# Performance work log

Hardware: AMD Instinct MI355X
Metric: run time of the kernel (lower is better)

Reference implementation:

```python
import jax, jax.numpy as jnp
import numpy as np

K = 3            # kernel_size
PAD = K // 2
CENTER_OFFSET = 0.0


def obb2offset(obb, stride):
    """obb: [N,5,H,W] (x_ctr,y_ctr,w,h,theta) in image coords -> deform offsets [N,2*K*K,H,W]."""
    N, _, H, W = obb.shape
    idx = jnp.arange(-PAD, PAD + 1, dtype=jnp.float32)
    yy, xx = jnp.meshgrid(idx, idx, indexing='ij')   # torch.meshgrid default 'ij'
    xx = xx.reshape(-1)                               # [KK]
    yy = yy.reshape(-1)
    x_ctr, y_ctr, w, h, a = [obb[:, i] for i in range(5)]   # each [N,H,W]
    s = jnp.float32(stride)
    x_ctr, y_ctr, w, h = x_ctr / s, y_ctr / s, w / s, h / s
    cos, sin = jnp.cos(a), jnp.sin(a)
    dw, dh = w / K, h / K
    px = dw[..., None] * xx                           # [N,H,W,KK]
    py = dh[..., None] * yy
    xr = cos[..., None] * px - sin[..., None] * py    # rotate kernel grid by theta
    yr = sin[..., None] * px + cos[..., None] * py
    x_anchor = xr + x_ctr[..., None]
    y_anchor = yr + y_ctr[..., None]
    xc = jnp.arange(W, dtype=jnp.float32)
    yc = jnp.arange(H, dtype=jnp.float32)
    x_conv = xc[None, None, :, None] + xx + CENTER_OFFSET   # [1,1,W,KK]
    y_conv = yc[None, :, None, None] + yy + CENTER_OFFSET   # [1,H,1,KK]
    off = jnp.stack([y_anchor - y_conv, x_anchor - x_conv], axis=-1)  # [N,H,W,KK,2]
    return off.reshape(N, H, W, 2 * K * K).transpose(0, 3, 1, 2)


def deform_conv(x, offsets, weight):
    """Deformable conv v1, zero padding, stride 1. x:[N,Cin,H,W], offsets:[N,2KK,H,W], weight:[Cout,Cin,K,K]."""
    N, Cin, H, W = x.shape
    KK = K * K
    Cout = weight.shape[0]
    off = offsets.reshape(N, KK, 2, H, W)
    dy, dx = off[:, :, 0], off[:, :, 1]                        # [N,KK,H,W]
    ky = jnp.arange(KK, dtype=jnp.float32) // K - PAD
    kx = jnp.arange(KK, dtype=jnp.float32) % K - PAD
    py = jnp.arange(H, dtype=jnp.float32)[None, None, :, None] + ky[None, :, None, None] + dy
    px = jnp.arange(W, dtype=jnp.float32)[None, None, None, :] + kx[None, :, None, None] + dx
    y0 = jnp.floor(py)
    x0 = jnp.floor(px)
    ly = py - y0                                               # bilinear fractions
    lx = px - x0
    y0i = y0.astype(jnp.int32)
    x0i = x0.astype(jnp.int32)
    x_flat = x.reshape(N, Cin, H * W)

    def corner(iy, ix):
        valid = (iy >= 0) & (iy < H) & (ix >= 0) & (ix < W)
        idx = jnp.clip(iy, 0, H - 1) * W + jnp.clip(ix, 0, W - 1)  # [N,KK,H,W]
        g = jax.vmap(lambda xf, ii: xf[:, ii.reshape(-1)].reshape(Cin, KK, H, W))(x_flat, idx)
        return jnp.where(valid[:, None], g, 0.0)               # [N,Cin,KK,H,W]

    v00 = corner(y0i, x0i)
    v01 = corner(y0i, x0i + 1)
    v10 = corner(y0i + 1, x0i)
    v11 = corner(y0i + 1, x0i + 1)
    wy = ly[:, None]
    wx = lx[:, None]
    sampled = (v00 * (1 - wy) * (1 - wx) + v01 * (1 - wy) * wx
               + v10 * wy * (1 - wx) + v11 * wy * wx)          # [N,Cin,KK,H,W]
    return jnp.einsum('nckhw,ock->nohw', sampled, weight.reshape(Cout, Cin, KK))


def setup_inputs() -> dict:
    key = jax.random.key(0)
    k1, k2, k3, k4, k5, k6 = jax.random.split(key, 6)
    N, Cin, Cout, H, W, stride = 2, 256, 256, 128, 128, 8
    x = jax.random.normal(k1, (N, Cin, H, W), jnp.float32)
    gy, gx = jnp.meshgrid(jnp.arange(H, dtype=jnp.float32), jnp.arange(W, dtype=jnp.float32), indexing='ij')
    xc = (gx[None] + jax.random.uniform(k2, (N, H, W), minval=-0.5, maxval=0.5)) * stride
    yc = (gy[None] + jax.random.uniform(k3, (N, H, W), minval=-0.5, maxval=0.5)) * stride
    wb = jax.random.uniform(k4, (N, H, W), minval=2.0 * stride, maxval=8.0 * stride)
    hb = jax.random.uniform(k5, (N, H, W), minval=2.0 * stride, maxval=8.0 * stride)
    th = jax.random.uniform(k6, (N, H, W), minval=-np.pi / 2, maxval=np.pi / 2)
    obb = jnp.stack([xc, yc, wb, hb, th], axis=1)              # [N,5,H,W]
    weight = jax.random.normal(jax.random.fold_in(key, 7), (Cout, Cin, K, K), jnp.float32) * 0.02
    return {"x": x, "obb": obb, "weight": weight, "stride": stride}


def reference(x, obb, weight, stride):
    offsets = obb2offset(jax.lax.stop_gradient(obb), stride)   # offsets.detach() in original
    return deform_conv(x, offsets, weight)
```

## Files before the change

### kernel.cpp

```cpp
#include <hip/hip_runtime.h>

#define HH 128
#define WW 128
#define CIN 256
#define COUT 256
#define KTOT 2304
#define HW (HH * WW)
#define NIT 36

typedef __attribute__((ext_vector_type(8))) short short8;
typedef __attribute__((ext_vector_type(4))) float f32x4;

__device__ __forceinline__ unsigned rne_bf16(float f) {
  unsigned u = __float_as_uint(f);
  return (u + 0x7FFFu + ((u >> 16) & 1u)) >> 16;
}
__device__ __forceinline__ unsigned pack_bf16x2(float lo, float hi) {
  return rne_bf16(lo) | (rne_bf16(hi) << 16);
}
__device__ __forceinline__ unsigned cvt_pk_bf16(float lo, float hi) {
  unsigned r;
  asm("v_cvt_pk_bf16_f32 %0, %1, %2" : "=v"(r) : "v"(lo), "v"(hi));
  return r;
}
__device__ __forceinline__ float bflo(unsigned u) { return __uint_as_float(u << 16); }
__device__ __forceinline__ float bfhi(unsigned u) { return __uint_as_float(u & 0xFFFF0000u); }

__device__ __forceinline__ unsigned blend2(unsigned a, unsigned b, unsigned c, unsigned d,
                                           float w00, float w01, float w10, float w11) {
  float lo = w00 * bflo(a) + w01 * bflo(b) + w10 * bflo(c) + w11 * bflo(d);
  float hi = w00 * bfhi(a) + w01 * bfhi(b) + w10 * bfhi(c) + w11 * bfhi(d);
  return cvt_pk_bf16(lo, hi);
}

__device__ __forceinline__ void glds16(const unsigned short* g, unsigned short* l) {
  __builtin_amdgcn_global_load_lds(
      (const __attribute__((address_space(1))) void*)g,
      (__attribute__((address_space(3))) void*)l, 16, 0, 0);
}

__global__ void prep_inputs(const float* __restrict__ x, const float* __restrict__ wsrc,
                            unsigned short* __restrict__ xt, unsigned short* __restrict__ wT) {
  int b = blockIdx.x;
  __shared__ float tile[64][129];
  if (b < 1024) {
    int cg = b & 3;
    int nh = b >> 2;
    int n = nh >> 7, h = nh & 127;
    int c0 = cg << 6;
    const float* xp = x + ((size_t)n * CIN * HH + h) * WW;
    for (int e = threadIdx.x; e < 64 * 128; e += 256) {
      int w = e & 127, ci = e >> 7;
      tile[ci][w] = xp[(size_t)(c0 + ci) * HW + w];
    }
    __syncthreads();
    unsigned* dst = (unsigned*)(xt + ((size_t)(n * HH + h) * WW) * CIN + c0);
    for (int e = threadIdx.x; e < 128 * 32; e += 256) {
      int w = e >> 5, cp = e & 31;
      dst[w * (CIN / 2) + cp] = pack_bf16x2(tile[2 * cp][w], tile[2 * cp + 1][w]);
    }
  } else {
    int o = (b - 1024) * 256 + threadIdx.x;
    if (o >= COUT * KTOT) return;
    int co = o / KTOT;
    int r = o - co * KTOT;
    int kk = r >> 8, ci = r & 255;
    wT[o] = rne_bf16(wsrc[(size_t)(co * CIN + ci) * 9 + kk]);
  }
}

__global__ __launch_bounds__(512, 2) void fused_deform_gemm(
    const float* __restrict__ obb, const unsigned short* __restrict__ xt,
    const unsigned short* __restrict__ wT, float* __restrict__ out,
    const int* __restrict__ stride_p) {
  int g = blockIdx.x;
  int xcd = g & 7, li = g >> 3;
  int u = xcd * 64 + li;
  int mh = u & 1;
  int bm = u >> 1;
  int n = bm >> 7, h = bm & 127;
  int tid = threadIdx.x;

  __shared__ __align__(16) unsigned short Alds[64 * 64];
  __shared__ __align__(16) unsigned short Blds[256 * 64];
  __shared__ float pcx[64], pcy[64], pA[64], pB[64], pC[64], pD[64];

  float inv_s = 1.0f / (float)stride_p[0];

  if (tid < 64) {
    int w = mh * 64 + tid;
    const float* op = obb + ((size_t)n * 5 * HH + h) * WW + w;
    float xc = op[0] * inv_s;
    float yc = op[(size_t)1 * HW] * inv_s;
    float bw = op[(size_t)2 * HW] * inv_s;
    float bh = op[(size_t)3 * HW] * inv_s;
    float th = op[(size_t)4 * HW];
    float sn, cs;
    sincosf(th, &sn, &cs);
    float dw = bw * (1.0f / 3.0f), dh = bh * (1.0f / 3.0f);
    pcx[tid] = xc; pcy[tid] = yc;
    pA[tid] = dw * cs; pB[tid] = dh * sn;
    pC[tid] = dw * sn; pD[tid] = dh * cs;
  }

  f32x4 acc[2][4] = {};

  int lane = tid & 63;
  int wv = tid >> 6;
  int wm = (wv & 1) * 32;
  int wn = (wv >> 1) * 64;
  int l15 = lane & 15, l4 = lane >> 4;

  int chunk8 = (lane & 7) * 8;
  int p = wv * 8 + (lane >> 3);
  int AldsOff = p * 128 + (((lane & 7) * 16) ^ ((p & 7) << 4));

  int cbl = ((lane & 7) * 16) ^ ((lane >> 3) << 4);
  int BsrcC[4];
  int BldsC[4];
#pragma unroll
  for (int t = 0; t < 4; ++t) {
    int row = t * 64 + wv * 8 + (lane >> 3);
    BsrcC[t] = row * (KTOT * 2) + cbl;
    BldsC[t] = (t * 64 + wv * 8) * 128;
  }

  int rdXor = (l15 & 7) << 4;
  int rc0 = (l4 * 16) ^ rdXor;
  int rc1 = (64 + l4 * 16) ^ rdXor;

  float wgt_[4];
  int boff[4];
  uint4 pf[4];
  uint4 aw;

  __syncthreads();

  auto prep = [&](int kk) {
    float fky = (float)(kk / 3 - 1);
    float fkx = (float)(kk % 3 - 1);
    float sx = pcx[p] + fkx * pA[p] - fky * pB[p];
    float sy = pcy[p] + fkx * pC[p] + fky * pD[p];
    float fx = floorf(sx), fy = floorf(sy);
    float lx = sx - fx, ly = sy - fy;
    int x0 = (int)fx, y0 = (int)fy;
    float vy0 = (y0 >= 0 && y0 < HH) ? 1.0f : 0.0f;
    float vy1 = (y0 >= -1 && y0 < HH - 1) ? 1.0f : 0.0f;
    float vx0 = (x0 >= 0 && x0 < WW) ? 1.0f : 0.0f;
    float vx1 = (x0 >= -1 && x0 < WW - 1) ? 1.0f : 0.0f;
    wgt_[0] = (1.0f - ly) * (1.0f - lx) * vy0 * vx0;
    wgt_[1] = (1.0f - ly) * lx * vy0 * vx1;
    wgt_[2] = ly * (1.0f - lx) * vy1 * vx0;
    wgt_[3] = ly * lx * vy1 * vx1;
    int xc0 = min(max(x0, 0), WW - 1), xc1 = min(max(x0 + 1, 0), WW - 1);
    int yc0 = min(max(y0, 0), HH - 1), yc1 = min(max(y0 + 1, 0), HH - 1);
    int rb0 = (n * HH + yc0) * WW, rb1 = (n * HH + yc1) * WW;
    boff[0] = (rb0 + xc0) * CIN;
    boff[1] = (rb0 + xc1) * CIN;
    boff[2] = (rb1 + xc0) * CIN;
    boff[3] = (rb1 + xc1) * CIN;
  };

  auto issueA = [&](int cc) {
    int co = cc * 64 + chunk8;
#pragma unroll
    for (int c = 0; c < 4; ++c)
      pf[c] = *(const uint4*)(xt + boff[c] + co);
  };

  auto blendA = [&]() {
    uint4 r;
    r.x = blend2(pf[0].x, pf[1].x, pf[2].x, pf[3].x, wgt_[0], wgt_[1], wgt_[2], wgt_[3]);
    r.y = blend2(pf[0].y, pf[1].y, pf[2].y, pf[3].y, wgt_[0], wgt_[1], wgt_[2], wgt_[3]);
    r.z = blend2(pf[0].z, pf[1].z, pf[2].z, pf[3].z, wgt_[0], wgt_[1], wgt_[2], wgt_[3]);
    r.w = blend2(pf[0].w, pf[1].w, pf[2].w, pf[3].w, wgt_[0], wgt_[1], wgt_[2], wgt_[3]);
    aw = r;
  };

  prep(0);
  issueA(0);
  blendA();
  issueA(1);

  char* AB = (char*)Alds;
  char* BB = (char*)Blds;

  for (int it = 0; it < NIT; ++it) {
    *(uint4*)(AB + AldsOff) = aw;
    {
      const unsigned short* wTit = wT + it * 64;
#pragma unroll
      for (int t = 0; t < 4; ++t)
        glds16((const unsigned short*)((const char*)wTit + BsrcC[t]),
               (unsigned short*)(BB + BldsC[t]));
    }
    asm volatile("s_waitcnt vmcnt(0) lgkmcnt(0)" ::: "memory");
    __builtin_amdgcn_s_barrier();
    asm volatile("" ::: "memory");

    int nx = it + 1;
    if (nx < NIT) {
      blendA();
      int nn = it + 2;
      if (nn < NIT) {
        if ((nn & 3) == 0) prep(nn >> 2);
        issueA(nn & 3);
      }
    }

#pragma unroll
    for (int ksi = 0; ksi < 2; ++ksi) {
      int rc = ksi ? rc1 : rc0;
      short8 af[2];
#pragma unroll
      for (int i = 0; i < 2; ++i)
        af[i] = *(const short8*)(AB + (wm + i * 16 + l15) * 128 + rc);
#pragma unroll
      for (int j = 0; j < 4; ++j) {
        short8 bf = *(const short8*)(BB + (wn + j * 16 + l15) * 128 + rc);
#pragma unroll
        for (int i = 0; i < 2; ++i)
          acc[i][j] = __builtin_amdgcn_mfma_f32_16x16x32_bf16(af[i], bf, acc[i][j], 0, 0, 0);
      }
    }
    asm volatile("s_waitcnt lgkmcnt(0)" ::: "memory");
    __builtin_amdgcn_s_barrier();
    asm volatile("" ::: "memory");
  }

  float* outp = out + (size_t)n * COUT * HW + (size_t)h * WW + mh * 64;
#pragma unroll
  for (int i = 0; i < 2; ++i) {
    int w0 = wm + i * 16 + l4 * 4;
#pragma unroll
    for (int j = 0; j < 4; ++j) {
      int co = wn + j * 16 + l15;
      *(f32x4*)(outp + (size_t)co * HW + w0) = acc[i][j];
    }
  }
}

extern "C" void kernel_launch(void* const* d_in, const int* in_sizes, int n_in,
                              void* d_out, int out_size, void* d_ws, size_t ws_size,
                              hipStream_t stream) {
  const float* x = (const float*)d_in[0];
  const float* obb = (const float*)d_in[1];
  const float* wgt = (const float*)d_in[2];
  const int* stridep = (const int*)d_in[3];
  float* out = (float*)d_out;

  unsigned short* xt = (unsigned short*)d_ws;
  unsigned short* wT = xt + (size_t)2 * HH * WW * CIN;

  prep_inputs<<<dim3(1024 + 2304), 256, 0, stream>>>(x, wgt, xt, wT);
  fused_deform_gemm<<<dim3(512), 512, 0, stream>>>(obb, xt, wT, out, stridep);
}
```

Measured before the change: 153.2 us.

## Load weights directly into MFMA registers and double-buffer A tile in LDS

Pre-permutes the bf16 weights into an MFMA fragment-ready layout so each wave loads its B operands straight from global memory into registers, with no LDS staging. This removes the B LDS buffer and one barrier per iteration. The A tile is double-buffered in LDS, per-pixel OBB parameters are kept in registers instead of shared memory, and the bilinear blend uses packed f32 FMA. Launch bounds are raised to 4 blocks, which trades register pressure and repeated global weight reads for higher occupancy and less synchronisation.

```diff
diff --git a/kernel.cpp b/kernel.cpp
--- a/kernel.cpp
+++ b/kernel.cpp
@@ -10,6 +10,7 @@
 
 typedef __attribute__((ext_vector_type(8))) short short8;
 typedef __attribute__((ext_vector_type(4))) float f32x4;
+typedef __attribute__((ext_vector_type(2))) float f32x2;
 
 __device__ __forceinline__ unsigned rne_bf16(float f) {
   unsigned u = __float_as_uint(f);
@@ -23,24 +24,25 @@
   asm("v_cvt_pk_bf16_f32 %0, %1, %2" : "=v"(r) : "v"(lo), "v"(hi));
   return r;
 }
-__device__ __forceinline__ float bflo(unsigned u) { return __uint_as_float(u << 16); }
-__device__ __forceinline__ float bfhi(unsigned u) { return __uint_as_float(u & 0xFFFF0000u); }
-
-__device__ __forceinline__ unsigned blend2(unsigned a, unsigned b, unsigned c, unsigned d,
-                                           float w00, float w01, float w10, float w11) {
-  float lo = w00 * bflo(a) + w01 * bflo(b) + w10 * bflo(c) + w11 * bflo(d);
-  float hi = w00 * bfhi(a) + w01 * bfhi(b) + w10 * bfhi(c) + w11 * bfhi(d);
-  return cvt_pk_bf16(lo, hi);
-}
-
-__device__ __forceinline__ void glds16(const unsigned short* g, unsigned short* l) {
-  __builtin_amdgcn_global_load_lds(
-      (const __attribute__((address_space(1))) void*)g,
-      (__attribute__((address_space(3))) void*)l, 16, 0, 0);
+__device__ __forceinline__ f32x2 up2(unsigned u) {
+  f32x2 r;
+  r.x = __uint_as_float(u << 16);
+  r.y = __uint_as_float(u & 0xFFFF0000u);
+  return r;
+}
+__device__ __forceinline__ f32x2 pkmul(f32x2 w, f32x2 v) {
+  f32x2 d;
+  asm("v_pk_mul_f32 %0, %1, %2" : "=v"(d) : "v"(w), "v"(v));
+  return d;
+}
+__device__ __forceinline__ f32x2 pkfma(f32x2 w, f32x2 v, f32x2 c) {
+  f32x2 d;
+  asm("v_pk_fma_f32 %0, %1, %2, %3" : "=v"(d) : "v"(w), "v"(v), "v"(c));
+  return d;
 }
 
 __global__ void prep_inputs(const float* __restrict__ x, const float* __restrict__ wsrc,
-                            unsigned short* __restrict__ xt, unsigned short* __restrict__ wT) {
+                            unsigned short* __restrict__ xt, unsigned short* __restrict__ wB) {
   int b = blockIdx.x;
   __shared__ float tile[64][129];
   if (b < 1024) {
@@ -65,13 +67,19 @@
     int co = o / KTOT;
     int r = o - co * KTOT;
     int kk = r >> 8, ci = r & 255;
-    wT[o] = rne_bf16(wsrc[(size_t)(co * CIN + ci) * 9 + kk]);
-  }
-}
-
-__global__ __launch_bounds__(512, 2) void fused_deform_gemm(
+    int it = r >> 6;
+    int rem = r & 63;
+    int ksi = rem >> 5;
+    int l4 = (rem >> 3) & 3;
+    int e = rem & 7;
+    int off = (it * 32 + (co >> 4) * 2 + ksi) * 512 + (l4 * 16 + (co & 15)) * 8 + e;
+    wB[off] = rne_bf16(wsrc[(size_t)(co * CIN + ci) * 9 + kk]);
+  }
+}
+
+__global__ __launch_bounds__(512, 4) void fused_deform_gemm(
     const float* __restrict__ obb, const unsigned short* __restrict__ xt,
-    const unsigned short* __restrict__ wT, float* __restrict__ out,
+    const unsigned short* __restrict__ wB, float* __restrict__ out,
     const int* __restrict__ stride_p) {
   int g = blockIdx.x;
   int xcd = g & 7, li = g >> 3;
@@ -81,14 +89,23 @@
   int n = bm >> 7, h = bm & 127;
   int tid = threadIdx.x;
 
-  __shared__ __align__(16) unsigned short Alds[64 * 64];
-  __shared__ __align__(16) unsigned short Blds[256 * 64];
-  __shared__ float pcx[64], pcy[64], pA[64], pB[64], pC[64], pD[64];
+  __shared__ __align__(16) unsigned short Alds[2][64 * 64];
 
   float inv_s = 1.0f / (float)stride_p[0];
 
-  if (tid < 64) {
-    int w = mh * 64 + tid;
+  int lane = tid & 63;
+  int wv = tid >> 6;
+  int wm = (wv & 1) * 32;
+  int wn = (wv >> 1) * 64;
+  int l15 = lane & 15, l4 = lane >> 4;
+
+  int chunk8 = (lane & 7) * 8;
+  int p = wv * 8 + (lane >> 3);
+  int AldsOff = p * 128 + (((lane & 7) * 16) ^ ((p & 7) << 4));
+
+  float cx_, cy_, pa_, pb_, pc_, pd_;
+  {
+    int w = mh * 64 + p;
     const float* op = obb + ((size_t)n * 5 * HH + h) * WW + w;
     float xc = op[0] * inv_s;
     float yc = op[(size_t)1 * HW] * inv_s;
@@ -98,49 +115,29 @@
     float sn, cs;
     sincosf(th, &sn, &cs);
     float dw = bw * (1.0f / 3.0f), dh = bh * (1.0f / 3.0f);
-    pcx[tid] = xc; pcy[tid] = yc;
-    pA[tid] = dw * cs; pB[tid] = dh * sn;
-    pC[tid] = dw * sn; pD[tid] = dh * cs;
+    cx_ = xc; cy_ = yc;
+    pa_ = dw * cs; pb_ = dh * sn;
+    pc_ = dw * sn; pd_ = dh * cs;
   }
 
   f32x4 acc[2][4] = {};
 
-  int lane = tid & 63;
-  int wv = tid >> 6;
-  int wm = (wv & 1) * 32;
-  int wn = (wv >> 1) * 64;
-  int l15 = lane & 15, l4 = lane >> 4;
-
-  int chunk8 = (lane & 7) * 8;
-  int p = wv * 8 + (lane >> 3);
-  int AldsOff = p * 128 + (((lane & 7) * 16) ^ ((p & 7) << 4));
-
-  int cbl = ((lane & 7) * 16) ^ ((lane >> 3) << 4);
-  int BsrcC[4];
-  int BldsC[4];
-#pragma unroll
-  for (int t = 0; t < 4; ++t) {
-    int row = t * 64 + wv * 8 + (lane >> 3);
-    BsrcC[t] = row * (KTOT * 2) + cbl;
-    BldsC[t] = (t * 64 + wv * 8) * 128;
-  }
+  const char* wBb = (const char*)wB + ((wv >> 1) * 4) * 2048 + lane * 16;
 
   int rdXor = (l15 & 7) << 4;
   int rc0 = (l4 * 16) ^ rdXor;
   int rc1 = (64 + l4 * 16) ^ rdXor;
 
-  float wgt_[4];
+  f32x2 wgt2[4];
   int boff[4];
   uint4 pf[4];
   uint4 aw;
 
-  __syncthreads();
-
   auto prep = [&](int kk) {
     float fky = (float)(kk / 3 - 1);
     float fkx = (float)(kk % 3 - 1);
-    float sx = pcx[p] + fkx * pA[p] - fky * pB[p];
-    float sy = pcy[p] + fkx * pC[p] + fky * pD[p];
+    float sx = cx_ + fkx * pa_ - fky * pb_;
+    float sy = cy_ + fkx * pc_ + fky * pd_;
     float fx = floorf(sx), fy = floorf(sy);
     float lx = sx - fx, ly = sy - fy;
     int x0 = (int)fx, y0 = (int)fy;
@@ -148,10 +145,14 @@
     float vy1 = (y0 >= -1 && y0 < HH - 1) ? 1.0f : 0.0f;
     float vx0 = (x0 >= 0 && x0 < WW) ? 1.0f : 0.0f;
     float vx1 = (x0 >= -1 && x0 < WW - 1) ? 1.0f : 0.0f;
-    wgt_[0] = (1.0f - ly) * (1.0f - lx) * vy0 * vx0;
-    wgt_[1] = (1.0f - ly) * lx * vy0 * vx1;
-    wgt_[2] = ly * (1.0f - lx) * vy1 * vx0;
-    wgt_[3] = ly * lx * vy1 * vx1;
+    float w00 = (1.0f - ly) * (1.0f - lx) * vy0 * vx0;
+    float w01 = (1.0f - ly) * lx * vy0 * vx1;
+    float w10 = ly * (1.0f - lx) * vy1 * vx0;
+    float w11 = ly * lx * vy1 * vx1;
+    wgt2[0] = (f32x2){w00, w00};
+    wgt2[1] = (f32x2){w01, w01};
+    wgt2[2] = (f32x2){w10, w10};
+    wgt2[3] = (f32x2){w11, w11};
     int xc0 = min(max(x0, 0), WW - 1), xc1 = min(max(x0 + 1, 0), WW - 1);
     int yc0 = min(max(y0, 0), HH - 1), yc1 = min(max(y0 + 1, 0), HH - 1);
     int rb0 = (n * HH + yc0) * WW, rb1 = (n * HH + yc1) * WW;
@@ -168,61 +169,70 @@
       pf[c] = *(const uint4*)(xt + boff[c] + co);
   };
 
+  auto blendW = [&](unsigned a, unsigned b, unsigned c, unsigned d) -> unsigned {
+    f32x2 s = pkmul(wgt2[0], up2(a));
+    s = pkfma(wgt2[1], up2(b), s);
+    s = pkfma(wgt2[2], up2(c), s);
+    s = pkfma(wgt2[3], up2(d), s);
+    return cvt_pk_bf16(s.x, s.y);
+  };
+
   auto blendA = [&]() {
     uint4 r;
-    r.x = blend2(pf[0].x, pf[1].x, pf[2].x, pf[3].x, wgt_[0], wgt_[1], wgt_[2], wgt_[3]);
-    r.y = blend2(pf[0].y, pf[1].y, pf[2].y, pf[3].y, wgt_[0], wgt_[1], wgt_[2], wgt_[3]);
-    r.z = blend2(pf[0].z, pf[1].z, pf[2].z, pf[3].z, wgt_[0], wgt_[1], wgt_[2], wgt_[3]);
-    r.w = blend2(pf[0].w, pf[1].w, pf[2].w, pf[3].w, wgt_[0], wgt_[1], wgt_[2], wgt_[3]);
+    r.x = blendW(pf[0].x, pf[1].x, pf[2].x, pf[3].x);
+    r.y = blendW(pf[0].y, pf[1].y, pf[2].y, pf[3].y);
+    r.z = blendW(pf[0].z, pf[1].z, pf[2].z, pf[3].z);
+    r.w = blendW(pf[0].w, pf[1].w, pf[2].w, pf[3].w);
     aw = r;
   };
+
+  char* AB = (char*)&Alds[0][0];
 
   prep(0);
   issueA(0);
   blendA();
+  *(uint4*)(AB + AldsOff) = aw;
   issueA(1);
-
-  char* AB = (char*)Alds;
-  char* BB = (char*)Blds;
+  asm volatile("s_waitcnt lgkmcnt(0)" ::: "memory");
+  __builtin_amdgcn_s_barrier();
+  asm volatile("" ::: "memory");
 
   for (int it = 0; it < NIT; ++it) {
-    *(uint4*)(AB + AldsOff) = aw;
-    {
-      const unsigned short* wTit = wT + it * 64;
-#pragma unroll
-      for (int t = 0; t < 4; ++t)
-        glds16((const unsigned short*)((const char*)wTit + BsrcC[t]),
-               (unsigned short*)(BB + BldsC[t]));
-    }
-    asm volatile("s_waitcnt vmcnt(0) lgkmcnt(0)" ::: "memory");
-    __builtin_amdgcn_s_barrier();
-    asm volatile("" ::: "memory");
-
-    int nx = it + 1;
-    if (nx < NIT) {
+    const char* bp = wBb + it * 32768;
+    short8 bf[8];
+#pragma unroll
+    for (int j = 0; j < 4; ++j) {
+      bf[j * 2 + 0] = *(const short8*)(bp + j * 2048);
+      bf[j * 2 + 1] = *(const short8*)(bp + j * 2048 + 1024);
+    }
+
+    if (it + 1 < NIT) {
       blendA();
-      int nn = it + 2;
-      if (nn < NIT) {
-        if ((nn & 3) == 0) prep(nn >> 2);
-        issueA(nn & 3);
+      *(uint4*)(AB + ((it + 1) & 1) * 8192 + AldsOff) = aw;
+      int t2 = it + 2;
+      if (t2 < NIT) {
+        if ((t2 & 3) == 0) prep(t2 >> 2);
+        issueA(t2 & 3);
       }
     }
 
+    char* ABr = AB + (it & 1) * 8192;
+    __builtin_amdgcn_s_setprio(1);
 #pragma unroll
     for (int ksi = 0; ksi < 2; ++ksi) {
       int rc = ksi ? rc1 : rc0;
       short8 af[2];
 #pragma unroll
       for (int i = 0; i < 2; ++i)
-        af[i] = *(const short8*)(AB + (wm + i * 16 + l15) * 128 + rc);
-#pragma unroll
-      for (int j = 0; j < 4; ++j) {
-        short8 bf = *(const short8*)(BB + (wn + j * 16 + l15) * 128 + rc);
+        af[i] = *(const short8*)(ABr + (wm + i * 16 + l15) * 128 + rc);
+#pragma unroll
+      for (int j = 0; j < 4; ++j)
 #pragma unroll
         for (int i = 0; i < 2; ++i)
-          acc[i][j] = __builtin_amdgcn_mfma_f32_16x16x32_bf16(af[i], bf, acc[i][j], 0, 0, 0);
-      }
-    }
+          acc[i][j] = __builtin_amdgcn_mfma_f32_16x16x32_bf16(af[i], bf[j * 2 + ksi], acc[i][j], 0, 0, 0);
+    }
+    __builtin_amdgcn_s_setprio(0);
+
     asm volatile("s_waitcnt lgkmcnt(0)" ::: "memory");
     __builtin_amdgcn_s_barrier();
     asm volatile("" ::: "memory");
@@ -250,8 +260,8 @@
   float* out = (float*)d_out;
 
   unsigned short* xt = (unsigned short*)d_ws;
-  unsigned short* wT = xt + (size_t)2 * HH * WW * CIN;
-
-  prep_inputs<<<dim3(1024 + 2304), 256, 0, stream>>>(x, wgt, xt, wT);
-  fused_deform_gemm<<<dim3(512), 512, 0, stream>>>(obb, xt, wT, out, stridep);
-}
+  unsigned short* wB = xt + (size_t)2 * HH * WW * CIN;
+
+  prep_inputs<<<dim3(1024 + 2304), 256, 0, stream>>>(x, wgt, xt, wB);
+  fused_deform_gemm<<<dim3(512), 512, 0, stream>>>(obb, xt, wB, out, stridep);
+}
```

After: 167.4 us. 9.3% more time.
